# Kernel tuning notes

Hardware: AMD Instinct MI355X
Metric: run time of the kernel (lower is better)

## Reference

```python
import jax, jax.numpy as jnp
import numpy as np

B = 524288  # batch size (number of ODE state samples)
D = 32      # state dimension (in_dim == out_dim forced by x.mm(weight) shape)


def setup_inputs() -> dict:
    key = jax.random.key(0)
    k1, k2, k3 = jax.random.split(key, 3)
    x = jax.random.normal(k1, (B, D), dtype=jnp.float32)
    # LinearODELayer weight, init uniform(-0.1, 0.1); used as x @ W_lin directly.
    W_lin = jax.random.uniform(k2, (D, D), dtype=jnp.float32, minval=-0.1, maxval=0.1)
    # NonLinearODELayer weight [D, D, D], init uniform(-0.001, 0.001).
    W_nl = jax.random.uniform(k3, (D, D, D), dtype=jnp.float32, minval=-0.001, maxval=0.001)
    return {"x": x, "W_lin": W_lin, "W_nl": W_nl}


def reference(x, W_lin, W_nl):
    # LinearODELayer: x.mm(weight) -> [B, D]
    lin = x @ W_lin
    # NonLinearODELayer: the matmul -> matmul(x.t()) -> permute -> diagonal -> t()
    # chain is exactly the batched bilinear form out[b, o] = x[b] @ W_nl[o] @ x[b].
    nl = jnp.einsum("bi,oij,bj->bo", x, W_nl, x)
    return lin + nl
```

## Files before the change

### kernel.cpp

```cpp
#include <hip/hip_runtime.h>


typedef __attribute__((ext_vector_type(8))) __bf16 bf16x8;
typedef __attribute__((ext_vector_type(4))) float floatx4;
typedef __attribute__((ext_vector_type(2))) float floatx2;

#define NB     524288
#define NCHUNK (NB / 32)
#define GRID   768
#define REDW   544

__device__ __forceinline__ int XW32(int r, int e) {
    return r * 32 + ((((e >> 2) ^ (r & 7)) << 2) | (e & 3));
}

__device__ __forceinline__ bf16x8 pack8(floatx4 a, floatx4 b) {
    bf16x8 f;
    #pragma unroll
    for (int j = 0; j < 4; ++j) { f[j] = (__bf16)a[j]; f[j + 4] = (__bf16)b[j]; }
    return f;
}

__global__ __launch_bounds__(256, 3)
void nnode_kernel(const float* __restrict__ x, const float* __restrict__ Wlin,
                  const float* __restrict__ Wnl, float* __restrict__ out) {
    __shared__ __align__(16) float xs[2][1024];
    __shared__ __align__(16) float red[2][2][2][REDW];

    const int tid  = threadIdx.x;
    const int wave = tid >> 6;
    const int lane = tid & 63;
    const int q    = lane >> 4;
    const int col  = lane & 15;
    const int tile = wave >> 1;
    const int w01  = wave & 1;

    bf16x8 bW[10][2];
    #pragma unroll
    for (int kl = 0; kl < 10; ++kl) {
        const int t  = w01 * 10 + kl;
        const int p  = t >> 1, h = t & 1;
        const int pa = (p < 4) ? 0 : ((p < 7) ? 1 : ((p < 9) ? 2 : 3));
        const int pb = p - ((p < 4) ? 0 : ((p < 7) ? 3 : ((p < 9) ? 5 : 6)));
        const int i1 = 8 * pa + 4 * h + q;
        #pragma unroll
        for (int tt = 0; tt < 2; ++tt) {
            const float* base = Wnl + (size_t)(col + 16 * tt) * 1024;
            floatx4 v0 = *(const floatx4*)(base + i1 * 32 + 8 * pb);
            floatx4 v1 = *(const floatx4*)(base + i1 * 32 + 8 * pb + 4);
            if (pa != pb) {
                #pragma unroll
                for (int j = 0; j < 4; ++j) {
                    v0[j] += base[(size_t)(8 * pb + j) * 32 + i1];
                    v1[j] += base[(size_t)(8 * pb + 4 + j) * 32 + i1];
                }
            }
            bW[kl][tt] = pack8(v0, v1);
        }
    }

    bf16x8 bl0, bl1;
    #pragma unroll
    for (int j = 0; j < 8; ++j) {
        bl0[j] = (__bf16)(0.5f * Wlin[(q * 8 + j) * 32 + col]);
        bl1[j] = (__bf16)(0.5f * Wlin[(q * 8 + j) * 32 + col + 16]);
    }

    const bool q1 = (q & 1) != 0;
    const bool q2 = (q & 2) != 0;

    const int sword = (tid >> 3) * 32 + (((tid & 7) ^ ((tid >> 3) & 7)) << 2);
    const int xrow  = tile * 16 + col;
    const int rT  = tid >> 7;
    const int rr  = (tid >> 3) & 15;
    const int rc4 = (tid & 7) * 4;

    const int n = 21 + ((blockIdx.x < (NCHUNK - 21 * GRID)) ? 1 : 0);

    {
        floatx4 v = *(const floatx4*)(x + (size_t)blockIdx.x * 1024 + tid * 4);
        *(floatx4*)&xs[0][sword] = v;
    }
    __syncthreads();

    int chunk = blockIdx.x;
    for (int k = 0; k < n; ++k, chunk += GRID) {
        const int cur = k & 1;

        floatx4 pre;
        if (k < n - 1)
            pre = *(const floatx4*)(x + (size_t)(chunk + GRID) * 1024 + tid * 4);

        const float* xb = xs[cur];
        floatx4 X[8];
        #pragma unroll
        for (int j = 0; j < 8; ++j)
            X[j] = *(const floatx4*)&xb[XW32(xrow, 4 * j)];

        floatx4 acc0 = {0.f, 0.f, 0.f, 0.f};
        floatx4 acc1 = {0.f, 0.f, 0.f, 0.f};

        #define SELQ(V) (q2 ? (q1 ? (V)[3] : (V)[2]) : (q1 ? (V)[1] : (V)[0]))

        {
            floatx4 la0 = q2 ? (q1 ? X[6] : X[4]) : (q1 ? X[2] : X[0]);
            floatx4 la1 = q2 ? (q1 ? X[7] : X[5]) : (q1 ? X[3] : X[1]);
            bf16x8 af = pack8(la0, la1);
            acc0 = __builtin_amdgcn_mfma_f32_16x16x32_bf16(af, bl0, acc0, 0, 0, 0);
            acc1 = __builtin_amdgcn_mfma_f32_16x16x32_bf16(af, bl1, acc1, 0, 0, 0);
        }

        #define STEP(A, B, H, KL) {                                             \
            const float sc = SELQ(X[2 * (A) + (H)]);                            \
            floatx4 p0 = sc * X[2 * (B)];                                       \
            floatx4 p1 = sc * X[2 * (B) + 1];                                   \
            bf16x8 af = pack8(p0, p1);                                          \
            acc0 = __builtin_amdgcn_mfma_f32_16x16x32_bf16(af, bW[KL][0], acc0, 0, 0, 0); \
            acc1 = __builtin_amdgcn_mfma_f32_16x16x32_bf16(af, bW[KL][1], acc1, 0, 0, 0); }

        if (w01 == 0) {
            STEP(0,0,0,0) STEP(0,0,1,1) STEP(0,1,0,2) STEP(0,1,1,3) STEP(0,2,0,4)
            STEP(0,2,1,5) STEP(0,3,0,6) STEP(0,3,1,7) STEP(1,1,0,8) STEP(1,1,1,9)
        } else {
            STEP(1,2,0,0) STEP(1,2,1,1) STEP(1,3,0,2) STEP(1,3,1,3) STEP(2,2,0,4)
            STEP(2,2,1,5) STEP(2,3,0,6) STEP(2,3,1,7) STEP(3,3,0,8) STEP(3,3,1,9)
        }
        #undef STEP
        #undef SELQ

        {
            float* rp = &red[cur][tile][w01][0];
            #pragma unroll
            for (int r2 = 0; r2 < 4; ++r2) {
                rp[(q * 4 + r2) * 34 + col]      = acc0[r2];
                rp[(q * 4 + r2) * 34 + col + 16] = acc1[r2];
            }
        }
        if (k < n - 1)
            *(floatx4*)&xs[cur ^ 1][sword] = pre;
        __syncthreads();

        {
            const float* b0p = &red[cur][rT][0][rr * 34 + rc4];
            const float* b1p = &red[cur][rT][1][rr * 34 + rc4];
            floatx2 u0 = *(const floatx2*)(b0p);
            floatx2 u1 = *(const floatx2*)(b0p + 2);
            floatx2 v0 = *(const floatx2*)(b1p);
            floatx2 v1 = *(const floatx2*)(b1p + 2);
            floatx4 s = {u0.x + v0.x, u0.y + v0.y, u1.x + v1.x, u1.y + v1.y};
            *(floatx4*)(out + ((size_t)chunk * 32 + rT * 16 + rr) * 32 + rc4) = s;
        }
    }
}

extern "C" void kernel_launch(void* const* d_in, const int* in_sizes, int n_in,
                              void* d_out, int out_size, void* d_ws, size_t ws_size,
                              hipStream_t stream) {
    const float* x    = (const float*)d_in[0];
    const float* Wlin = (const float*)d_in[1];
    const float* Wnl  = (const float*)d_in[2];
    float* out        = (float*)d_out;
    nnode_kernel<<<dim3(GRID), dim3(256), 0, stream>>>(x, Wlin, Wnl, out);
}
```

Measured before the change: 188.9 us.

## Halve chunk size and split output columns across waves instead of row tiles

Processes 16-row chunks instead of 32, with each wave pair splitting the 32 output columns into halves rather than splitting rows into two tiles. This halves the bf16 weight fragments held per thread and the LDS footprint, which may reduce register pressure. In exchange, each packed A operand now feeds one MFMA instead of two, so packing/scaling VALU work, LDS reads and barriers per output row double, and global accesses narrow to 8-byte vectors.

```diff
diff --git a/kernel.cpp b/kernel.cpp
--- a/kernel.cpp
+++ b/kernel.cpp
@@ -6,11 +6,11 @@
 typedef __attribute__((ext_vector_type(2))) float floatx2;
 
 #define NB     524288
-#define NCHUNK (NB / 32)
+#define NCHUNK (NB / 16)
 #define GRID   768
 #define REDW   544
 
-__device__ __forceinline__ int XW32(int r, int e) {
+__device__ __forceinline__ int XW(int r, int e) {
     return r * 32 + ((((e >> 2) ^ (r & 7)) << 2) | (e & 3));
 }
 
@@ -24,18 +24,18 @@
 __global__ __launch_bounds__(256, 3)
 void nnode_kernel(const float* __restrict__ x, const float* __restrict__ Wlin,
                   const float* __restrict__ Wnl, float* __restrict__ out) {
-    __shared__ __align__(16) float xs[2][1024];
-    __shared__ __align__(16) float red[2][2][2][REDW];
+    __shared__ __align__(16) float xs[2][512];
+    __shared__ __align__(16) float red[2][2][REDW];
 
     const int tid  = threadIdx.x;
     const int wave = tid >> 6;
     const int lane = tid & 63;
     const int q    = lane >> 4;
     const int col  = lane & 15;
-    const int tile = wave >> 1;
-    const int w01  = wave & 1;
+    const int half = wave & 1;
+    const int w01  = wave >> 1;
 
-    bf16x8 bW[10][2];
+    bf16x8 bW[10];
     #pragma unroll
     for (int kl = 0; kl < 10; ++kl) {
         const int t  = w01 * 10 + kl;
@@ -43,43 +43,35 @@
         const int pa = (p < 4) ? 0 : ((p < 7) ? 1 : ((p < 9) ? 2 : 3));
         const int pb = p - ((p < 4) ? 0 : ((p < 7) ? 3 : ((p < 9) ? 5 : 6)));
         const int i1 = 8 * pa + 4 * h + q;
-        #pragma unroll
-        for (int tt = 0; tt < 2; ++tt) {
-            const float* base = Wnl + (size_t)(col + 16 * tt) * 1024;
-            floatx4 v0 = *(const floatx4*)(base + i1 * 32 + 8 * pb);
-            floatx4 v1 = *(const floatx4*)(base + i1 * 32 + 8 * pb + 4);
-            if (pa != pb) {
-                #pragma unroll
-                for (int j = 0; j < 4; ++j) {
-                    v0[j] += base[(size_t)(8 * pb + j) * 32 + i1];
-                    v1[j] += base[(size_t)(8 * pb + 4 + j) * 32 + i1];
-                }
+        const float* base = Wnl + (size_t)(col + 16 * half) * 1024;
+        floatx4 v0 = *(const floatx4*)(base + i1 * 32 + 8 * pb);
+        floatx4 v1 = *(const floatx4*)(base + i1 * 32 + 8 * pb + 4);
+        if (pa != pb) {
+            #pragma unroll
+            for (int j = 0; j < 4; ++j) {
+                v0[j] += base[(size_t)(8 * pb + j) * 32 + i1];
+                v1[j] += base[(size_t)(8 * pb + 4 + j) * 32 + i1];
             }
-            bW[kl][tt] = pack8(v0, v1);
         }
+        bW[kl] = pack8(v0, v1);
     }
 
-    bf16x8 bl0, bl1;
+    bf16x8 bl;
     #pragma unroll
-    for (int j = 0; j < 8; ++j) {
-        bl0[j] = (__bf16)(0.5f * Wlin[(q * 8 + j) * 32 + col]);
-        bl1[j] = (__bf16)(0.5f * Wlin[(q * 8 + j) * 32 + col + 16]);
-    }
+    for (int j = 0; j < 8; ++j)
+        bl[j] = (__bf16)(0.5f * Wlin[(q * 8 + j) * 32 + 16 * half + col]);
 
     const bool q1 = (q & 1) != 0;
     const bool q2 = (q & 2) != 0;
 
-    const int sword = (tid >> 3) * 32 + (((tid & 7) ^ ((tid >> 3) & 7)) << 2);
-    const int xrow  = tile * 16 + col;
-    const int rT  = tid >> 7;
-    const int rr  = (tid >> 3) & 15;
-    const int rc4 = (tid & 7) * 4;
+    const int srow  = tid >> 4;
+    const int scol2 = (tid & 15) * 2;
 
-    const int n = 21 + ((blockIdx.x < (NCHUNK - 21 * GRID)) ? 1 : 0);
+    const int n = 42 + ((blockIdx.x < (NCHUNK - 42 * GRID)) ? 1 : 0);
 
     {
-        floatx4 v = *(const floatx4*)(x + (size_t)blockIdx.x * 1024 + tid * 4);
-        *(floatx4*)&xs[0][sword] = v;
+        floatx2 v = *(const floatx2*)(x + (size_t)blockIdx.x * 512 + tid * 2);
+        *(floatx2*)&xs[0][XW(srow, scol2)] = v;
     }
     __syncthreads();
 
@@ -87,18 +79,17 @@
     for (int k = 0; k < n; ++k, chunk += GRID) {
         const int cur = k & 1;
 
-        floatx4 pre;
+        floatx2 pre;
         if (k < n - 1)
-            pre = *(const floatx4*)(x + (size_t)(chunk + GRID) * 1024 + tid * 4);
+            pre = *(const floatx2*)(x + (size_t)(chunk + GRID) * 512 + tid * 2);
 
         const float* xb = xs[cur];
         floatx4 X[8];
         #pragma unroll
         for (int j = 0; j < 8; ++j)
-            X[j] = *(const floatx4*)&xb[XW32(xrow, 4 * j)];
+            X[j] = *(const floatx4*)&xb[XW(col, 4 * j)];
 
-        floatx4 acc0 = {0.f, 0.f, 0.f, 0.f};
-        floatx4 acc1 = {0.f, 0.f, 0.f, 0.f};
+        floatx4 acc = {0.f, 0.f, 0.f, 0.f};
 
         #define SELQ(V) (q2 ? (q1 ? (V)[3] : (V)[2]) : (q1 ? (V)[1] : (V)[0]))
 
@@ -106,8 +97,7 @@
             floatx4 la0 = q2 ? (q1 ? X[6] : X[4]) : (q1 ? X[2] : X[0]);
             floatx4 la1 = q2 ? (q1 ? X[7] : X[5]) : (q1 ? X[3] : X[1]);
             bf16x8 af = pack8(la0, la1);
-            acc0 = __builtin_amdgcn_mfma_f32_16x16x32_bf16(af, bl0, acc0, 0, 0, 0);
-            acc1 = __builtin_amdgcn_mfma_f32_16x16x32_bf16(af, bl1, acc1, 0, 0, 0);
+            acc = __builtin_amdgcn_mfma_f32_16x16x32_bf16(af, bl, acc, 0, 0, 0);
         }
 
         #define STEP(A, B, H, KL) {                                             \
@@ -115,8 +105,7 @@
             floatx4 p0 = sc * X[2 * (B)];                                       \
             floatx4 p1 = sc * X[2 * (B) + 1];                                   \
             bf16x8 af = pack8(p0, p1);                                          \
-            acc0 = __builtin_amdgcn_mfma_f32_16x16x32_bf16(af, bW[KL][0], acc0, 0, 0, 0); \
-            acc1 = __builtin_amdgcn_mfma_f32_16x16x32_bf16(af, bW[KL][1], acc1, 0, 0, 0); }
+            acc = __builtin_amdgcn_mfma_f32_16x16x32_bf16(af, bW[KL], acc, 0, 0, 0); }
 
         if (w01 == 0) {
             STEP(0,0,0,0) STEP(0,0,1,1) STEP(0,1,0,2) STEP(0,1,1,3) STEP(0,2,0,4)
@@ -129,26 +118,22 @@
         #undef SELQ
 
         {
-            float* rp = &red[cur][tile][w01][0];
+            float* rp = &red[cur][w01][0];
             #pragma unroll
-            for (int r2 = 0; r2 < 4; ++r2) {
-                rp[(q * 4 + r2) * 34 + col]      = acc0[r2];
-                rp[(q * 4 + r2) * 34 + col + 16] = acc1[r2];
-            }
+            for (int r2 = 0; r2 < 4; ++r2)
+                rp[(q * 4 + r2) * 34 + 16 * half + col] = acc[r2];
         }
         if (k < n - 1)
-            *(floatx4*)&xs[cur ^ 1][sword] = pre;
+            *(floatx2*)&xs[cur ^ 1][XW(srow, scol2)] = pre;
         __syncthreads();
 
         {
-            const float* b0p = &red[cur][rT][0][rr * 34 + rc4];
-            const float* b1p = &red[cur][rT][1][rr * 34 + rc4];
-            floatx2 u0 = *(const floatx2*)(b0p);
-            floatx2 u1 = *(const floatx2*)(b0p + 2);
-            floatx2 v0 = *(const floatx2*)(b1p);
-            floatx2 v1 = *(const floatx2*)(b1p + 2);
-            floatx4 s = {u0.x + v0.x, u0.y + v0.y, u1.x + v1.x, u1.y + v1.y};
-            *(floatx4*)(out + ((size_t)chunk * 32 + rT * 16 + rr) * 32 + rc4) = s;
+            const float* rb0 = &red[cur][0][srow * 34 + scol2];
+            const float* rb1 = &red[cur][1][srow * 34 + scol2];
+            floatx2 a = *(const floatx2*)rb0;
+            floatx2 b = *(const floatx2*)rb1;
+            floatx2 s = {a.x + b.x, a.y + b.y};
+            *(floatx2*)(out + (size_t)chunk * 512 + tid * 2) = s;
         }
     }
 }
```

New measurement: 170.7 us. 1.11x faster.
